# Performance work log

Hardware: AMD Instinct MI355X
Metric: run time of the kernel (lower is better)

Reference implementation:

```python
import jax, jax.numpy as jnp
import numpy as np

N_NODES = 60000
N_HERB = 5000
N_PROT = 20000
PROT_OFFSET = N_HERB  # proteins follow herbs in the flattened node ordering
DIM = 128
N_REL = 6
N_BASES = 30
N_EDGES = 600000
N_PAIRS = 40000
HIDDEN = DIM


def setup_inputs() -> dict:
    key = jax.random.key(0)
    ks = jax.random.split(key, 16)
    inp = {}
    inp["edge_index"] = jax.random.randint(ks[0], (2, N_EDGES), 0, N_NODES)
    inp["edge_type"] = jax.random.randint(ks[1], (N_EDGES,), 0, N_REL)
    inp["h_idx"] = jax.random.randint(ks[2], (N_PAIRS,), 0, N_HERB)
    inp["p_idx"] = jax.random.randint(ks[3], (N_PAIRS,), 0, N_PROT)
    # learned node embeddings (all node types use nn.Embedding here)
    inp["node_emb"] = jax.random.normal(ks[4], (N_NODES, DIM), jnp.float32) * 0.1
    # RGCN layer 1 (basis decomposition + root + bias, as in PyG RGCNConv)
    inp["basis1"] = jax.random.normal(ks[5], (N_BASES, DIM, DIM), jnp.float32) * 0.05
    inp["comp1"] = jax.random.normal(ks[6], (N_REL, N_BASES), jnp.float32) * 0.1
    inp["root1"] = jax.random.normal(ks[7], (DIM, DIM), jnp.float32) * 0.05
    inp["bias1"] = jnp.zeros((DIM,), jnp.float32)
    # RGCN layer 2
    inp["basis2"] = jax.random.normal(ks[8], (N_BASES, DIM, DIM), jnp.float32) * 0.05
    inp["comp2"] = jax.random.normal(ks[9], (N_REL, N_BASES), jnp.float32) * 0.1
    inp["root2"] = jax.random.normal(ks[10], (DIM, DIM), jnp.float32) * 0.05
    inp["bias2"] = jnp.zeros((DIM,), jnp.float32)
    # scorer MLP: Linear(4*dim, hidden) -> ReLU -> Linear(hidden, 1)
    inp["sw1"] = jax.random.normal(ks[11], (4 * DIM, HIDDEN), jnp.float32) * 0.05
    inp["sb1"] = jnp.zeros((HIDDEN,), jnp.float32)
    inp["sw2"] = jax.random.normal(ks[12], (HIDDEN, 1), jnp.float32) * 0.05
    inp["sb2"] = jnp.zeros((1,), jnp.float32)
    return inp


def _rgcn_layer(x, edge_index, edge_type, basis, comp, root, bias):
    """PyG RGCNConv with basis decomposition, aggr='mean', root weight + bias.

    out[i] = sum_r mean_{j in N_r(i)} x_j @ W_r + x_i @ root + bias,
    with W_r = sum_b comp[r,b] * basis[b]. Because messages are linear, we
    aggregate (mean) per (dst, relation) first, then apply W_r once per node.
    """
    N, D = x.shape
    R = comp.shape[0]
    src, dst = edge_index[0], edge_index[1]
    seg = dst * R + edge_type  # segment per (destination, relation)
    sums = jax.ops.segment_sum(x[src], seg, num_segments=N * R)       # [N*R, D]
    cnt = jax.ops.segment_sum(jnp.ones_like(edge_type, dtype=x.dtype), seg,
                              num_segments=N * R)                      # [N*R]
    mean = (sums / jnp.maximum(cnt, 1.0)[:, None]).reshape(N, R, D)    # [N, R, D]
    W = jnp.einsum('rb,bdo->rdo', comp, basis)                         # [R, D, D]
    out = jnp.einsum('nrd,rdo->no', mean, W)
    return out + x @ root + bias


def reference(edge_index, edge_type, h_idx, p_idx, node_emb,
              basis1, comp1, root1, bias1,
              basis2, comp2, root2, bias2,
              sw1, sb1, sw2, sb2):
    x = _rgcn_layer(node_emb, edge_index, edge_type, basis1, comp1, root1, bias1)
    x = jax.nn.relu(x)
    # dropout omitted (eval mode)
    x = _rgcn_layer(x, edge_index, edge_type, basis2, comp2, root2, bias2)
    h = x[h_idx]                       # herbs occupy global ids [0, N_HERB)
    p = x[PROT_OFFSET + p_idx]         # proteins follow herbs
    feat = jnp.concatenate([h, p, h * p, jnp.abs(h - p)], axis=-1)  # [P, 4D]
    hid = jax.nn.relu(feat @ sw1 + sb1)
    return (hid @ sw2 + sb2).reshape(-1)
```

## Files before the change

### kernel.cpp

```cpp
#include <hip/hip_runtime.h>
#include <hip/hip_bf16.h>
#include <cstdint>

#define DIMX   128
#define N_REL  6
#define N_BASES 30
#define N_HERB 5000
#define NWIDE  896
#define YW     768
#define KSC    512
#define BN     64
#define KT     16

typedef __attribute__((ext_vector_type(8))) short short8v;
typedef __attribute__((ext_vector_type(4))) float f32x4;

__device__ __forceinline__ unsigned short f2bf_rne(float f) {
    union { float f; unsigned u; } v; v.f = f;
    unsigned u = v.u;
    u += 0x7fffu + ((u >> 16) & 1u);
    return (unsigned short)(u >> 16);
}
__device__ __forceinline__ float bf2f(unsigned short h) {
    union { unsigned u; float f; } v; v.u = ((unsigned)h) << 16;
    return v.f;
}


__global__ void k_count(const int* __restrict__ ei, const int* __restrict__ et,
                        int E, int* __restrict__ cnt) {
    int e = blockIdx.x * blockDim.x + threadIdx.x;
    if (e >= E) return;
    int dst = ei[E + e];
    int t   = et[e];
    atomicAdd(&cnt[dst * N_REL + t], 1);
}

__global__ void k_invcnt(const int* __restrict__ cnt, float* __restrict__ inv, int n) {
    int i = blockIdx.x * blockDim.x + threadIdx.x;
    if (i >= n) return;
    int c = cnt[i];
    inv[i] = 1.0f / (float)(c > 0 ? c : 1);
}

__global__ void k_deg(const int* __restrict__ cnt, int* __restrict__ deg, int n) {
    int i = blockIdx.x * blockDim.x + threadIdx.x;
    if (i >= n) return;
    int s = 0;
    #pragma unroll
    for (int t = 0; t < N_REL; ++t) s += cnt[i * N_REL + t];
    deg[i] = s;
}


__global__ void k_scan1(const int* __restrict__ deg, int* __restrict__ bsums, int n) {
    __shared__ int ssum[256];
    int tid = threadIdx.x;
    int base = blockIdx.x * 1024;
    int local = 0;
    #pragma unroll
    for (int i = 0; i < 4; ++i) {
        int idx = base + tid * 4 + i;
        local += (idx < n) ? deg[idx] : 0;
    }
    ssum[tid] = local; __syncthreads();
    for (int off = 128; off; off >>= 1) {
        if (tid < off) ssum[tid] += ssum[tid + off];
        __syncthreads();
    }
    if (tid == 0) bsums[blockIdx.x] = ssum[0];
}

__global__ void k_scan2(int* __restrict__ bsums, int nb, int* __restrict__ rowptr, int n) {
    if (threadIdx.x == 0 && blockIdx.x == 0) {
        int run = 0;
        for (int b = 0; b < nb; ++b) { int t = bsums[b]; bsums[b] = run; run += t; }
        rowptr[n] = run;
    }
}

__global__ void k_scan3(const int* __restrict__ deg, const int* __restrict__ bsums,
                        int* __restrict__ rowptr, int n) {
    __shared__ int ssum[256];
    int tid = threadIdx.x;
    int base = blockIdx.x * 1024;
    int idx0 = base + tid * 4;
    int v[4]; int local = 0;
    #pragma unroll
    for (int i = 0; i < 4; ++i) {
        int idx = idx0 + i;
        v[i] = (idx < n) ? deg[idx] : 0;
        local += v[i];
    }
    ssum[tid] = local; __syncthreads();
    for (int off = 1; off < 256; off <<= 1) {
        int t = (tid >= off) ? ssum[tid - off] : 0;
        __syncthreads();
        ssum[tid] += t;
        __syncthreads();
    }
    int excl = ssum[tid] - local + bsums[blockIdx.x];
    #pragma unroll
    for (int i = 0; i < 4; ++i) {
        int idx = idx0 + i;
        if (idx < n) { rowptr[idx] = excl; excl += v[i]; }
    }
}

__global__ void k_fill(const int* __restrict__ ei, const int* __restrict__ et, int E,
                       const int* __restrict__ rowptr, int* __restrict__ fillc,
                       int* __restrict__ pedge) {
    int e = blockIdx.x * blockDim.x + threadIdx.x;
    if (e >= E) return;
    int src = ei[e];
    int dst = ei[E + e];
    int t   = et[e];
    int pos = atomicAdd(&fillc[dst], 1);
    pedge[rowptr[dst] + pos] = (src << 3) | t;
}


__global__ void k_buildW2(const float* __restrict__ basis, const float* __restrict__ comp,
                          const float* __restrict__ root, unsigned short* __restrict__ W2) {
    int d = blockIdx.x;
    int r = blockIdx.y;
    int o = threadIdx.x;
    float v;
    if (r < N_REL) {
        float acc = 0.f;
        #pragma unroll
        for (int b = 0; b < N_BASES; ++b)
            acc += comp[r * N_BASES + b] * basis[((size_t)b * DIMX + d) * DIMX + o];
        v = acc;
    } else {
        v = root[(size_t)d * DIMX + o];
    }
    unsigned short hi = f2bf_rne(v);
    unsigned short lo = f2bf_rne(v - bf2f(hi));
    size_t og = (size_t)(r * DIMX + o);
    W2[og * 256 + d] = hi;
    W2[og * 256 + 128 + d] = lo;
}


__global__ __launch_bounds__(256)
void k_prepA(const float* __restrict__ x, unsigned short* __restrict__ A2,
             int NN, int relu) {
    int row = blockIdx.x * 16 + (threadIdx.x >> 4);
    int c8  = (threadIdx.x & 15) * 8;
    float v[8];
    bool ok = (row < NN);
    if (ok) {
        float4 a = *(const float4*)(x + (size_t)row * DIMX + c8);
        float4 b = *(const float4*)(x + (size_t)row * DIMX + c8 + 4);
        v[0]=a.x; v[1]=a.y; v[2]=a.z; v[3]=a.w;
        v[4]=b.x; v[5]=b.y; v[6]=b.z; v[7]=b.w;
        if (relu) {
            #pragma unroll
            for (int i = 0; i < 8; ++i) v[i] = fmaxf(v[i], 0.f);
        }
    }
    __syncthreads();
    if (ok) {
        unsigned short hi[8], lo[8];
        #pragma unroll
        for (int i = 0; i < 8; ++i) {
            hi[i] = f2bf_rne(v[i]);
            lo[i] = f2bf_rne(v[i] - bf2f(hi[i]));
        }
        unsigned short* base = A2 + (size_t)row * 256;
        *(ulonglong2*)(base + c8)       = *(ulonglong2*)hi;
        *(ulonglong2*)(base + 128 + c8) = *(ulonglong2*)lo;
    }
}


__global__ __launch_bounds__(256)
void k_gemm_mfma(const unsigned short* __restrict__ A2, const unsigned short* __restrict__ W2,
                 const float* __restrict__ bias, float* __restrict__ y,
                 float* __restrict__ outbuf, int NN) {
    int tid = threadIdx.x;
    int w  = tid >> 6;
    int l  = tid & 63;
    int cl = l & 15;
    int kg = (l >> 4) * 8;
    int cb = blockIdx.y;
    int m0 = blockIdx.x * 64 + w * 16;

    int rowA = m0 + cl; if (rowA >= NN) rowA = NN - 1;
    const unsigned short* aBase = A2 + (size_t)rowA * 256 + kg;
    const unsigned short* bBase = W2 + (size_t)(cb * DIMX + cl) * 256 + kg;

    f32x4 acc[8];
    #pragma unroll
    for (int j = 0; j < 8; ++j) acc[j] = (f32x4){0.f, 0.f, 0.f, 0.f};

    #pragma unroll
    for (int k0 = 0; k0 < 128; k0 += 32) {
        short8v ah = *(const short8v*)(aBase + k0);
        short8v al = *(const short8v*)(aBase + 128 + k0);
        #pragma unroll
        for (int j = 0; j < 8; ++j) {
            const unsigned short* bp = bBase + (size_t)j * 16 * 256;
            short8v bh = *(const short8v*)(bp + k0);
            short8v bl = *(const short8v*)(bp + 128 + k0);
            acc[j] = __builtin_amdgcn_mfma_f32_16x16x32_bf16(ah, bh, acc[j], 0, 0, 0);
            acc[j] = __builtin_amdgcn_mfma_f32_16x16x32_bf16(al, bh, acc[j], 0, 0, 0);
            acc[j] = __builtin_amdgcn_mfma_f32_16x16x32_bf16(ah, bl, acc[j], 0, 0, 0);
        }
    }

    int rq = (l >> 4) * 4;
    if (cb < N_REL) {
        #pragma unroll
        for (int j = 0; j < 8; ++j) {
            #pragma unroll
            for (int q = 0; q < 4; ++q) {
                int n = m0 + rq + q;
                if (n < NN)
                    y[(size_t)n * YW + cb * DIMX + j * 16 + cl] = acc[j][q];
            }
        }
    } else {
        #pragma unroll
        for (int j = 0; j < 8; ++j) {
            float bv = bias[j * 16 + cl];
            #pragma unroll
            for (int q = 0; q < 4; ++q) {
                int n = m0 + rq + q;
                if (n < NN)
                    outbuf[(size_t)n * DIMX + j * 16 + cl] = acc[j][q] + bv;
            }
        }
    }
}


__global__ __launch_bounds__(256)
void k_gather(const int* __restrict__ pedge, const int* __restrict__ rowptr,
              const float* __restrict__ invc, const float* __restrict__ y,
              float* __restrict__ outbuf, int NN) {
    int wid = (blockIdx.x * blockDim.x + threadIdx.x) >> 6;
    if (wid >= NN) return;
    int lane = threadIdx.x & 63;
    int dst = wid;
    int j0 = rowptr[dst], j1 = rowptr[dst + 1];

    float* op = outbuf + (size_t)dst * DIMX + lane * 2;
    float2 acc = *(float2*)op;

    int j = j0;
    for (; j + 1 < j1; j += 2) {
        int pa = pedge[j], pb = pedge[j + 1];
        int ta = pa & 7, tb = pb & 7;
        int sa = pa >> 3, sb = pb >> 3;
        float fa = invc[dst * N_REL + ta];
        float fb = invc[dst * N_REL + tb];
        float2 va = *(const float2*)(y + (size_t)sa * YW + ta * DIMX + lane * 2);
        float2 vb = *(const float2*)(y + (size_t)sb * YW + tb * DIMX + lane * 2);
        acc.x += va.x * fa + vb.x * fb;
        acc.y += va.y * fa + vb.y * fb;
    }
    if (j < j1) {
        int pa = pedge[j];
        int ta = pa & 7;
        int sa = pa >> 3;
        float fa = invc[dst * N_REL + ta];
        float2 va = *(const float2*)(y + (size_t)sa * YW + ta * DIMX + lane * 2);
        acc.x += va.x * fa;
        acc.y += va.y * fa;
    }
    *(float2*)op = acc;
}


__global__ __launch_bounds__(256)
void k_scorer_gemm(const float* __restrict__ x2, const int* __restrict__ h_idx,
                   const int* __restrict__ p_idx, const float* __restrict__ sw1,
                   const float* __restrict__ sb1, float* __restrict__ hid, int P) {
    __shared__ float As[BN][KT];
    __shared__ float Ws[KT][DIMX];
    int tid = threadIdx.x;
    int n0 = blockIdx.x * BN;

    int lrow = tid >> 2;
    int lk4  = (tid & 3) * 4;
    int ng = n0 + lrow; if (ng >= P) ng = P - 1;
    int hrow = h_idx[ng];
    int prow = N_HERB + p_idx[ng];

    int oc = (tid & 31) * 4;
    int nb = (tid >> 5) * 8;

    float acc[8][4];
    #pragma unroll
    for (int i = 0; i < 8; ++i)
        #pragma unroll
        for (int j = 0; j < 4; ++j) acc[i][j] = 0.f;

    for (int k0 = 0; k0 < KSC; k0 += KT) {
        int k = k0 + lk4;
        int q = k >> 7;
        int d = k & 127;
        float4 hv = *(const float4*)(x2 + (size_t)hrow * DIMX + d);
        float4 pv = *(const float4*)(x2 + (size_t)prow * DIMX + d);
        float4 av;
        if (q == 0)      av = hv;
        else if (q == 1) av = pv;
        else if (q == 2) { av.x = hv.x * pv.x; av.y = hv.y * pv.y;
                           av.z = hv.z * pv.z; av.w = hv.w * pv.w; }
        else             { av.x = fabsf(hv.x - pv.x); av.y = fabsf(hv.y - pv.y);
                           av.z = fabsf(hv.z - pv.z); av.w = fabsf(hv.w - pv.w); }
        *(float4*)&As[lrow][lk4] = av;

        const float4* wsrc = (const float4*)(sw1 + (size_t)k0 * DIMX);
        ((float4*)Ws)[tid]       = wsrc[tid];
        ((float4*)Ws)[tid + 256] = wsrc[tid + 256];
        __syncthreads();

        #pragma unroll
        for (int kk = 0; kk < KT; kk += 4) {
            float4 wv0 = *(float4*)&Ws[kk + 0][oc];
            float4 wv1 = *(float4*)&Ws[kk + 1][oc];
            float4 wv2 = *(float4*)&Ws[kk + 2][oc];
            float4 wv3 = *(float4*)&Ws[kk + 3][oc];
            #pragma unroll
            for (int i = 0; i < 8; ++i) {
                float4 a4 = *(float4*)&As[nb + i][kk];
                acc[i][0] += a4.x * wv0.x + a4.y * wv1.x + a4.z * wv2.x + a4.w * wv3.x;
                acc[i][1] += a4.x * wv0.y + a4.y * wv1.y + a4.z * wv2.y + a4.w * wv3.y;
                acc[i][2] += a4.x * wv0.z + a4.y * wv1.z + a4.z * wv2.z + a4.w * wv3.z;
                acc[i][3] += a4.x * wv0.w + a4.y * wv1.w + a4.z * wv2.w + a4.w * wv3.w;
            }
        }
        __syncthreads();
    }

    float4 bv = *(const float4*)(sb1 + oc);
    #pragma unroll
    for (int i = 0; i < 8; ++i) {
        int n = n0 + nb + i;
        if (n < P) {
            float4 r;
            r.x = fmaxf(acc[i][0] + bv.x, 0.f);
            r.y = fmaxf(acc[i][1] + bv.y, 0.f);
            r.z = fmaxf(acc[i][2] + bv.z, 0.f);
            r.w = fmaxf(acc[i][3] + bv.w, 0.f);
            *(float4*)(hid + (size_t)n * DIMX + oc) = r;
        }
    }
}


__global__ void k_scorer_out(const float* __restrict__ hid, const float* __restrict__ sw2,
                             const float* __restrict__ sb2, float* __restrict__ out, int P) {
    int tid = blockIdx.x * blockDim.x + threadIdx.x;
    int wave = tid >> 6;
    int lane = tid & 63;
    int half = lane >> 5, l32 = lane & 31;
    int pair = wave * 2 + half;
    if (pair >= P) return;
    float4 hv = *(const float4*)(hid + (size_t)pair * DIMX + l32 * 4);
    float4 wv = *(const float4*)(sw2 + l32 * 4);
    float s = hv.x * wv.x + hv.y * wv.y + hv.z * wv.z + hv.w * wv.w;
    #pragma unroll
    for (int off = 16; off; off >>= 1) s += __shfl_xor(s, off, 64);
    if (l32 == 0) out[pair] = s + sb2[0];
}


extern "C" void kernel_launch(void* const* d_in, const int* in_sizes, int n_in,
                              void* d_out, int out_size, void* d_ws, size_t ws_size,
                              hipStream_t stream) {
    const int*   ei       = (const int*)d_in[0];
    const int*   et       = (const int*)d_in[1];
    const int*   h_idx    = (const int*)d_in[2];
    const int*   p_idx    = (const int*)d_in[3];
    const float* node_emb = (const float*)d_in[4];
    const float* basis1   = (const float*)d_in[5];
    const float* comp1    = (const float*)d_in[6];
    const float* root1    = (const float*)d_in[7];
    const float* bias1    = (const float*)d_in[8];
    const float* basis2   = (const float*)d_in[9];
    const float* comp2    = (const float*)d_in[10];
    const float* root2    = (const float*)d_in[11];
    const float* bias2    = (const float*)d_in[12];
    const float* sw1      = (const float*)d_in[13];
    const float* sb1      = (const float*)d_in[14];
    const float* sw2      = (const float*)d_in[15];
    const float* sb2      = (const float*)d_in[16];
    float* out = (float*)d_out;

    int E  = in_sizes[1];
    int P  = in_sizes[2];
    int NN = in_sizes[4] / DIMX;

    float* y      = (float*)d_ws;
    float* hid    = y;
    int*   cnt    = (int*)(y + (size_t)NN * YW);
    float* invc   = (float*)(cnt + (size_t)NN * N_REL);
    float* out1   = invc + (size_t)NN * N_REL;
    float* out2   = out1 + (size_t)NN * DIMX;
    unsigned short* W2 = (unsigned short*)(out2 + (size_t)NN * DIMX);
    int*   deg    = (int*)(W2 + (size_t)NWIDE * 256);
    int*   rowptr = deg + NN;
    int*   fillc  = rowptr + NN + 1;
    int*   bsums  = fillc + NN;
    int*   pedge  = bsums + 64;

    unsigned short* A2_l1 = (unsigned short*)out2;
    unsigned short* A2_l2 = (unsigned short*)out1;

    int nScanB = (NN + 1023) / 1024;

    hipMemsetAsync(cnt, 0, (size_t)NN * N_REL * sizeof(int), stream);
    hipMemsetAsync(fillc, 0, (size_t)NN * sizeof(int), stream);

    k_count<<<(E + 255) / 256, 256, 0, stream>>>(ei, et, E, cnt);
    k_invcnt<<<(NN * N_REL + 255) / 256, 256, 0, stream>>>(cnt, invc, NN * N_REL);
    k_deg<<<(NN + 255) / 256, 256, 0, stream>>>(cnt, deg, NN);
    k_scan1<<<nScanB, 256, 0, stream>>>(deg, bsums, NN);
    k_scan2<<<1, 64, 0, stream>>>(bsums, nScanB, rowptr, NN);
    k_scan3<<<nScanB, 256, 0, stream>>>(deg, bsums, rowptr, NN);
    k_fill<<<(E + 255) / 256, 256, 0, stream>>>(ei, et, E, rowptr, fillc, pedge);

    dim3 gemmGrid((NN + 63) / 64, N_REL + 1);
    dim3 wGrid(DIMX, N_REL + 1);
    int prepBlocks = (NN + 15) / 16;
    int gatherBlocks = ((size_t)NN * 64 + 255) / 256;

    k_buildW2<<<wGrid, DIMX, 0, stream>>>(basis1, comp1, root1, W2);
    k_prepA<<<prepBlocks, 256, 0, stream>>>(node_emb, A2_l1, NN, 0);
    k_gemm_mfma<<<gemmGrid, 256, 0, stream>>>(A2_l1, W2, bias1, y, out1, NN);
    k_gather<<<gatherBlocks, 256, 0, stream>>>(pedge, rowptr, invc, y, out1, NN);

    k_buildW2<<<wGrid, DIMX, 0, stream>>>(basis2, comp2, root2, W2);
    k_prepA<<<prepBlocks, 256, 0, stream>>>(out1, A2_l2, NN, 1);
    k_gemm_mfma<<<gemmGrid, 256, 0, stream>>>(A2_l2, W2, bias2, y, out2, NN);
    k_gather<<<gatherBlocks, 256, 0, stream>>>(pedge, rowptr, invc, y, out2, NN);

    k_scorer_gemm<<<(P + BN - 1) / BN, 256, 0, stream>>>(out2, h_idx, p_idx, sw1, sb1, hid, P);
    k_scorer_out<<<((size_t)P * 32 + 255) / 256, 256, 0, stream>>>(hid, sw2, sb2, out, P);
}
```

Baseline: 903.8 us.

## Keep weight fragments in registers and split output columns across waves

```diff
diff --git a/kernel.cpp b/kernel.cpp
--- a/kernel.cpp
+++ b/kernel.cpp
@@ -185,51 +185,56 @@
     int cl = l & 15;
     int kg = (l >> 4) * 8;
     int cb = blockIdx.y;
-    int m0 = blockIdx.x * 64 + w * 16;
-
-    int rowA = m0 + cl; if (rowA >= NN) rowA = NN - 1;
-    const unsigned short* aBase = A2 + (size_t)rowA * 256 + kg;
-    const unsigned short* bBase = W2 + (size_t)(cb * DIMX + cl) * 256 + kg;
-
-    f32x4 acc[8];
-    #pragma unroll
-    for (int j = 0; j < 8; ++j) acc[j] = (f32x4){0.f, 0.f, 0.f, 0.f};
-
-    #pragma unroll
-    for (int k0 = 0; k0 < 128; k0 += 32) {
-        short8v ah = *(const short8v*)(aBase + k0);
-        short8v al = *(const short8v*)(aBase + 128 + k0);
+    int rowBase = blockIdx.x * 64;
+    if (rowBase >= NN) return;
+    int nt = (NN - rowBase) >> 4; if (nt > 4) nt = 4;
+
+    int ocol0 = w * 32;
+    const unsigned short* bB0 = W2 + (size_t)(cb * DIMX + ocol0 + cl) * 256 + kg;
+    const unsigned short* bB1 = bB0 + 16 * 256;
+
+    short8v b0h[4], b0l[4], b1h[4], b1l[4];
+    #pragma unroll
+    for (int k0 = 0; k0 < 4; ++k0) {
+        b0h[k0] = *(const short8v*)(bB0 + k0 * 32);
+        b0l[k0] = *(const short8v*)(bB0 + 128 + k0 * 32);
+        b1h[k0] = *(const short8v*)(bB1 + k0 * 32);
+        b1l[k0] = *(const short8v*)(bB1 + 128 + k0 * 32);
+    }
+
+    int rq = (l >> 4) * 4;
+
+    for (int t = 0; t < nt; ++t) {
+        int r0 = rowBase + t * 16;
+        const unsigned short* aB = A2 + (size_t)(r0 + cl) * 256 + kg;
+        f32x4 acc0 = (f32x4){0.f, 0.f, 0.f, 0.f};
+        f32x4 acc1 = (f32x4){0.f, 0.f, 0.f, 0.f};
         #pragma unroll
-        for (int j = 0; j < 8; ++j) {
-            const unsigned short* bp = bBase + (size_t)j * 16 * 256;
-            short8v bh = *(const short8v*)(bp + k0);
-            short8v bl = *(const short8v*)(bp + 128 + k0);
-            acc[j] = __builtin_amdgcn_mfma_f32_16x16x32_bf16(ah, bh, acc[j], 0, 0, 0);
-            acc[j] = __builtin_amdgcn_mfma_f32_16x16x32_bf16(al, bh, acc[j], 0, 0, 0);
-            acc[j] = __builtin_amdgcn_mfma_f32_16x16x32_bf16(ah, bl, acc[j], 0, 0, 0);
-        }
-    }
-
-    int rq = (l >> 4) * 4;
-    if (cb < N_REL) {
-        #pragma unroll
-        for (int j = 0; j < 8; ++j) {
+        for (int k0 = 0; k0 < 4; ++k0) {
+            short8v ah = *(const short8v*)(aB + k0 * 32);
+            short8v al = *(const short8v*)(aB + 128 + k0 * 32);
+            acc0 = __builtin_amdgcn_mfma_f32_16x16x32_bf16(ah, b0h[k0], acc0, 0, 0, 0);
+            acc0 = __builtin_amdgcn_mfma_f32_16x16x32_bf16(al, b0h[k0], acc0, 0, 0, 0);
+            acc0 = __builtin_amdgcn_mfma_f32_16x16x32_bf16(ah, b0l[k0], acc0, 0, 0, 0);
+            acc1 = __builtin_amdgcn_mfma_f32_16x16x32_bf16(ah, b1h[k0], acc1, 0, 0, 0);
+            acc1 = __builtin_amdgcn_mfma_f32_16x16x32_bf16(al, b1h[k0], acc1, 0, 0, 0);
+            acc1 = __builtin_amdgcn_mfma_f32_16x16x32_bf16(ah, b1l[k0], acc1, 0, 0, 0);
+        }
+        if (cb < N_REL) {
+            float* yb = y + (size_t)(r0 + rq) * YW + cb * DIMX + ocol0 + cl;
             #pragma unroll
             for (int q = 0; q < 4; ++q) {
-                int n = m0 + rq + q;
-                if (n < NN)
-                    y[(size_t)n * YW + cb * DIMX + j * 16 + cl] = acc[j][q];
+                yb[(size_t)q * YW]      = acc0[q];
+                yb[(size_t)q * YW + 16] = acc1[q];
             }
-        }
-    } else {
-        #pragma unroll
-        for (int j = 0; j < 8; ++j) {
-            float bv = bias[j * 16 + cl];
+        } else {
+            float bv0 = bias[ocol0 + cl];
+            float bv1 = bias[ocol0 + 16 + cl];
+            float* ob = outbuf + (size_t)(r0 + rq) * DIMX + ocol0 + cl;
             #pragma unroll
             for (int q = 0; q < 4; ++q) {
-                int n = m0 + rq + q;
-                if (n < NN)
-                    outbuf[(size_t)n * DIMX + j * 16 + cl] = acc[j][q] + bv;
+                ob[(size_t)q * DIMX]      = acc0[q] + bv0;
+                ob[(size_t)q * DIMX + 16] = acc1[q] + bv1;
             }
         }
     }
```

Measured after the change: 736.7 us. 18.5% less time.
